# Optimization experiments

Hardware: AMD Instinct MI355X
Metric: run time of the kernel (lower is better)

The kernel has to match this reference:

```python
import jax, jax.numpy as jnp
import numpy as np

H = 4  # num_heads

def _ln(x, g, b):
    m = x.mean(-1, keepdims=True)
    v = ((x - m) ** 2).mean(-1, keepdims=True)
    return (x - m) * jax.lax.rsqrt(v + 1e-5) * g + b

def _mlp(x, w1, b1, w2, b2):
    return jax.nn.relu(x @ w1 + b1) @ w2 + b2

def _lin_att(q, k, v):
    # q,k,v: [BB, L, H, hd] ; linear (kernelized) attention, no softmax
    L = q.shape[1]
    qn = q / jnp.maximum(jnp.linalg.norm(q, axis=-1, keepdims=True), 1e-12)
    kn = k / jnp.maximum(jnp.linalg.norm(k, axis=-1, keepdims=True), 1e-12)
    kvs = jnp.einsum('blhm,blhd->bhmd', kn, v)
    num = jnp.einsum('bnhm,bhmd->bnhd', qn, kvs) + L * v
    den = jnp.einsum('bnhm,bhm->bnh', qn, kn.sum(axis=1))[..., None] + L
    return num / den

def _fast_attn(x4, w_qkv, w_op, b_op):
    # x4: [B,T,N,D]; spatial attention over N, temporal attention over T, concat, project
    B, T, N, D = x4.shape
    hd = D // H
    q, k, v = jnp.split(x4 @ w_qkv, 3, axis=-1)
    sh = lambda t: t.reshape(B * T, N, H, hd)
    out_s = _lin_att(sh(q), sh(k), sh(v)).reshape(B, T, N, D)
    th = lambda t: jnp.swapaxes(t, 1, 2).reshape(B * N, T, H, hd)
    out_t = jnp.swapaxes(_lin_att(th(q), th(k), th(v)).reshape(B, N, T, D), 1, 2)
    return jnp.concatenate([out_s, out_t], axis=-1) @ w_op + b_op

def _forward(x, W_in, b_in, adp, W_tp, b_tp, qkv_w, op_w, op_b, pw_w, pw_b,
             fc_w1, fc_b1, fc_w2, fc_b2, ln1_g, ln1_b, ln2_g, ln2_b,
             ep_w, ep_b, enc_w1, enc_b1, enc_w2, enc_b2, out_w, out_b):
    Nn, T, _ = x.shape
    xt = jnp.swapaxes(x, 0, 1)[None]                 # [1,T,N,in]
    h = xt @ W_in + b_in                             # input_proj -> [1,T,N,24]
    h = jnp.concatenate([h, adp[None]], axis=-1)     # + adaptive emb -> [1,T,N,104]
    h = h @ W_tp + b_tp                              # temporal_proj: 1x1 conv == pointwise linear
    graph = jnp.einsum('tnd,tmd->tnm', adp, adp)     # [T,N,N]
    graph = jax.nn.softmax(jax.nn.relu(graph), axis=-1)  # AvgPool(1,1) is identity
    # GraphPropagate (order=2, eval/no-dropout): [h, graph @ h]
    z1 = jnp.einsum('tni,btid->btnd', graph, h)
    att0 = _fast_attn(h, qkv_w[0], op_w[0], op_b[0])
    att1 = _fast_attn(z1, qkv_w[1], op_w[1], op_b[1])
    # scale = [1, 0.01]; note torch's in-place aliasing makes ln1 input = 2*x_glo
    g = h + att0 * (h @ pw_w[0] + pw_b[0]) + 0.01 * att1 * (att0 @ pw_w[1] + pw_b[1])
    h1 = _ln(2.0 * g, ln1_g, ln1_b)
    h2 = _ln(h1 + _mlp(h1, fc_w1, fc_b1, fc_w2, fc_b2), ln2_g, ln2_b)
    y = jnp.swapaxes(h2, 1, 2).reshape(1, Nn, T * h2.shape[-1]) @ ep_w + ep_b  # encoder_proj
    for i in range(enc_w1.shape[0]):                 # 3 residual MLP blocks
        y = y + _mlp(y, enc_w1[i], enc_b1[i], enc_w2[i], enc_b2[i])
    out = y @ out_w + out_b                          # [1,N,365]
    return out.reshape(Nn, T, 1)

def setup_inputs() -> dict:
    key = jax.random.key(0)
    ks = jax.random.split(key, 24)
    f = lambda i, shape, s=0.05: jax.random.normal(ks[i], shape, dtype=jnp.float32) * s
    D, T, N, IN = 104, 365, 400, 3
    return {
        'x': jax.random.normal(ks[0], (N, T, IN), dtype=jnp.float32),
        'W_in': f(1, (IN, 24)), 'b_in': f(2, (24,)),
        'adp': f(3, (T, N, 80)),
        'W_tp': f(4, (D, D)), 'b_tp': f(5, (D,)),
        'qkv_w': f(6, (2, D, 3 * D)),
        'op_w': f(7, (2, 2 * D, D)), 'op_b': f(8, (2, D)),
        'pw_w': f(9, (2, D, D)), 'pw_b': f(10, (2, D)),
        'fc_w1': f(11, (D, 2 * D)), 'fc_b1': f(12, (2 * D,)),
        'fc_w2': f(13, (2 * D, D)), 'fc_b2': f(14, (D,)),
        'ln1_g': jnp.ones((D,), jnp.float32), 'ln1_b': jnp.zeros((D,), jnp.float32),
        'ln2_g': jnp.ones((D,), jnp.float32), 'ln2_b': jnp.zeros((D,), jnp.float32),
        'ep_w': f(15, (T * D, D), 0.01), 'ep_b': f(16, (D,)),
        'enc_w1': f(17, (3, D, 2 * D)), 'enc_b1': f(18, (3, 2 * D)),
        'enc_w2': f(19, (3, 2 * D, D)), 'enc_b2': f(20, (3, D)),
        'out_w': f(21, (D, T)), 'out_b': f(22, (T,)),
    }

def reference(x, W_in, b_in, adp, W_tp, b_tp, qkv_w, op_w, op_b, pw_w, pw_b,
              fc_w1, fc_b1, fc_w2, fc_b2, ln1_g, ln1_b, ln2_g, ln2_b,
              ep_w, ep_b, enc_w1, enc_b1, enc_w2, enc_b2, out_w, out_b):
    return _forward(x, W_in, b_in, adp, W_tp, b_tp, qkv_w, op_w, op_b, pw_w, pw_b,
                    fc_w1, fc_b1, fc_w2, fc_b2, ln1_g, ln1_b, ln2_g, ln2_b,
                    ep_w, ep_b, enc_w1, enc_b1, enc_w2, enc_b2, out_w, out_b)
```

## Files before the change

kernel.cpp:

```cpp
#include <hip/hip_runtime.h>
#include <hip/hip_bf16.h>
#include <cstddef>

#define TT   365
#define NN   400
#define TN   (TT*NN)
#define HD   26
#define NH   4

#define CEILDIV(a,b) (((a)+(b)-1)/(b))

typedef __hip_bfloat16 bf16;
typedef short short8v __attribute__((ext_vector_type(8)));
typedef float float4v __attribute__((ext_vector_type(4)));
typedef float float16v __attribute__((ext_vector_type(16)));
__device__ __forceinline__ float b2f(bf16 v){ return __bfloat162float(v); }
__device__ __forceinline__ bf16  f2b(float v){ return __float2bfloat16(v); }

static constexpr size_t NB0 = (size_t)TN*104;
static constexpr size_t NB1 = (size_t)TN*104;
static constexpr size_t NB2 = (size_t)TN*312;
static constexpr size_t NB3 = (size_t)TN*104;
static constexpr size_t NBF = NB0+NB1+NB2+NB3;
static constexpr size_t NTILE   = (size_t)108*32;
static constexpr size_t NKVSB_S = (size_t)TT*NTILE;
static constexpr size_t NKVSB_T = (size_t)NN*NTILE;
static constexpr size_t NY      = (size_t)NN*104;
static constexpr size_t NW_TP   = 104*128;
static constexpr size_t NW_QKV  = 312*128;
static constexpr size_t NW_OP   = 104*224;
static constexpr size_t NW_PW   = 104*128;
static constexpr size_t NW_FC1  = 208*128;
static constexpr size_t NW_FC2  = 104*224;
static constexpr size_t NW_EPT  = (size_t)104*37960;
static constexpr size_t NWT     = NW_TP + 2*NW_QKV + 2*NW_OP + 2*NW_PW + NW_FC1 + NW_FC2 + NW_EPT;
static constexpr size_t WS_NEEDED = NBF*2 + (NKVSB_S+NKVSB_T)*2 + NY*4 + NWT*2;
static constexpr size_t NADP_ROWS = (size_t)TN + 64;
static constexpr size_t NADP = NADP_ROWS*96;
static constexpr size_t NHT  = ((size_t)TT*104 + 8)*448;
static_assert(NADP + NHT <= NB2, "z1 scratch must fit in B2");

__global__ void __launch_bounds__(256) prep_w(
    const float* __restrict__ W, bf16* __restrict__ Wt, int K, int Nc, int KP)
{
    int idx = blockIdx.x*256 + threadIdx.x;
    if (idx >= Nc*KP) return;
    int n = idx / KP, k = idx - n*KP;
    Wt[idx] = (k < K) ? f2b(W[(size_t)k*Nc + n]) : f2b(0.f);
}

__global__ void __launch_bounds__(256) prep_wT(
    const float* __restrict__ W, bf16* __restrict__ Wt)
{
    __shared__ float T[64][105];
    int k0 = blockIdx.x * 64;
    int tid = threadIdx.x;
    for (int idx = tid; idx < 64*104; idx += 256) {
        int r = idx / 104, c = idx - r*104;
        int k = k0 + r;
        T[r][c] = (k < 37960) ? W[(size_t)k*104 + c] : 0.f;
    }
    __syncthreads();
    for (int idx = tid; idx < 104*32; idx += 256) {
        int n = idx >> 5, kp = idx & 31;
        int k = kp*2;
        if (k0 + k + 1 < 37960 || k0 + k < 37960) {
            if (k0 + k < 37960) {
                bf16 lo = f2b(T[k][n]);
                bf16 hi = f2b(T[k+1][n]);
                uint v = ((uint)(*(ushort*)&hi) << 16) | (*(ushort*)&lo);
                if (k0 + k + 1 < 37960) *(uint*)(Wt + (size_t)n*37960 + k0 + k) = v;
                else Wt[(size_t)n*37960 + k0 + k] = lo;
            }
        }
    }
}

__global__ void __launch_bounds__(256) prep_adp(
    const float* __restrict__ adp, bf16* __restrict__ out)
{
    size_t i = (size_t)blockIdx.x*256 + threadIdx.x;
    if (i >= NADP) return;
    size_t row = i / 96; int e = (int)(i - row*96);
    float v = (row < TN && e < 80) ? adp[row*80 + e] : 0.f;
    out[i] = f2b(v);
}

__global__ void __launch_bounds__(256) ht_kernel(
    const bf16* __restrict__ h, bf16* __restrict__ hT)
{
    __shared__ bf16 As[64*106];
    int t = blockIdx.y, n0 = blockIdx.x*64;
    int tid = threadIdx.x;
    for (int idx = tid; idx < 64*52; idx += 256) {
        int r = idx / 52, k = idx - r*52;
        int n = n0 + r;
        uint v = 0;
        if (n < NN) v = *(const uint*)(h + ((size_t)t*NN + n)*104 + k*2);
        *(uint*)(&As[r*106 + k*2]) = v;
    }
    __syncthreads();
    for (int idx = tid; idx < 104*32; idx += 256) {
        int d = idx >> 5, np = idx & 31;
        int n = np*2;
        ushort lo = *(ushort*)&As[n*106 + d];
        ushort hi = *(ushort*)&As[(n+1)*106 + d];
        uint v = ((uint)hi << 16) | lo;
        *(uint*)(hT + ((size_t)t*104 + d)*448 + n0 + n) = v;
    }
}

__global__ void __launch_bounds__(128) hcat_kernel(
    const float* __restrict__ x, const float* __restrict__ W_in,
    const float* __restrict__ b_in, const float* __restrict__ adp,
    bf16* __restrict__ hcat)
{
    int bid = blockIdx.x;
    int t = bid / NN, n = bid - t*NN;
    int tid = threadIdx.x;
    if (tid < 24) {
        float s = b_in[tid];
        size_t xb = ((size_t)n*TT + t)*3;
        #pragma unroll
        for (int i = 0; i < 3; ++i) s += x[xb + i] * W_in[i*24 + tid];
        hcat[(size_t)bid*104 + tid] = f2b(s);
    } else if (tid < 104) {
        hcat[(size_t)bid*104 + tid] = f2b(adp[(size_t)bid*80 + (tid - 24)]);
    }
}

template<int KP>
__global__ void __launch_bounds__(256) gemm_mf(
    const bf16* __restrict__ A, int lda, int K,
    const bf16* __restrict__ Wt, const float* __restrict__ bias,
    bf16* __restrict__ C, int M, int Nc, int relu)
{
    constexpr int STR = KP + 8;
    constexpr int KPQ = KP/8;
    __shared__ bf16 As[64*STR];
    __shared__ bf16 Ws[64*STR];
    int nCol = (Nc + 63) >> 6;
    int nwg = gridDim.x;
    int bid = blockIdx.x;
    int xcd = bid & 7, kk = bid >> 3;
    int q8 = nwg >> 3, r8 = nwg & 7;
    int widx = (xcd < r8 ? xcd*(q8+1) : r8*(q8+1) + (xcd - r8)*q8) + kk;
    int mblk = widx / nCol;
    int m0 = mblk * 64;
    int c0 = (widx - mblk*nCol) * 64;
    int tid = threadIdx.x;
    const int KQ = K/8;
    uint4 z4 = {0u,0u,0u,0u};
    for (int idx = tid; idx < 64*KPQ; idx += 256) {
        int r = idx / KPQ, q = idx - r*KPQ;
        int m = m0 + r;
        uint4 v = z4;
        if (m < M && q < KQ) v = *(const uint4*)(A + (size_t)m*lda + q*8);
        *(uint4*)(&As[r*STR + q*8]) = v;
    }
    for (int idx = tid; idx < 64*KPQ; idx += 256) {
        int r = idx / KPQ, q = idx - r*KPQ;
        int n = c0 + r;
        uint4 v = z4;
        if (n < Nc) v = *(const uint4*)(Wt + (size_t)n*KP + q*8);
        *(uint4*)(&Ws[r*STR + q*8]) = v;
    }
    __syncthreads();

    int lane = tid & 63, w = tid >> 6;
    int n16 = lane & 15, quad = lane >> 4;
    constexpr int KS = KP/32;
    short8v af[KS];
    #pragma unroll
    for (int s = 0; s < KS; ++s)
        af[s] = *(const short8v*)(&As[(16*w + n16)*STR + s*32 + quad*8]);
    float4v acc[4];
    #pragma unroll
    for (int ct = 0; ct < 4; ++ct) { float4v z = {0.f,0.f,0.f,0.f}; acc[ct] = z; }
    #pragma unroll
    for (int ct = 0; ct < 4; ++ct) {
        #pragma unroll
        for (int s = 0; s < KS; ++s) {
            short8v bfr = *(const short8v*)(&Ws[(ct*16 + n16)*STR + s*32 + quad*8]);
            acc[ct] = __builtin_amdgcn_mfma_f32_16x16x32_bf16(af[s], bfr, acc[ct], 0, 0, 0);
        }
    }
    #pragma unroll
    for (int ct = 0; ct < 4; ++ct) {
        int c = c0 + ct*16 + n16;
        if (c < Nc) {
            float b = bias ? bias[c] : 0.f;
            #pragma unroll
            for (int reg = 0; reg < 4; ++reg) {
                int m = m0 + 16*w + quad*4 + reg;
                if (m < M) {
                    float v = acc[ct][reg] + b;
                    if (relu) v = fmaxf(v, 0.f);
                    C[(size_t)m*Nc + c] = f2b(v);
                }
            }
        }
    }
}

__global__ void __launch_bounds__(256) gate_ln1(
    bf16* __restrict__ h, const bf16* __restrict__ att0, const bf16* __restrict__ att1,
    const bf16* __restrict__ w0t, const bf16* __restrict__ w1t, const float* __restrict__ pwb,
    const float* __restrict__ gamma, const float* __restrict__ beta)
{
    constexpr int STR = 136;
    __shared__ bf16 A0s[64*STR];
    __shared__ bf16 A1s[64*STR];
    __shared__ bf16 Ws[112*STR];
    __shared__ float prm[416];
    int m0 = blockIdx.x * 64;
    int tid = threadIdx.x;
    int lane = tid & 63, w = tid >> 6, n16 = lane & 15, quad = lane >> 4;
    uint4 z4 = {0u,0u,0u,0u};

    for (int idx = tid; idx < 64*16; idx += 256) {
        int r = idx >> 4, q = idx & 15;
        int m = m0 + r;
        uint4 v0 = z4, v1 = z4;
        if (m < TN && q < 13) {
            v0 = *(const uint4*)(h    + (size_t)m*104 + q*8);
            v1 = *(const uint4*)(att0 + (size_t)m*104 + q*8);
        }
        *(uint4*)(&A0s[r*STR + q*8]) = v0;
        *(uint4*)(&A1s[r*STR + q*8]) = v1;
    }
    for (int idx = tid; idx < 112*16; idx += 256) {
        int c = idx >> 4, q = idx & 15;
        uint4 v = z4;
        if (c < 104) v = *(const uint4*)(w0t + (size_t)c*128 + q*8);
        *(uint4*)(&Ws[c*STR + q*8]) = v;
    }
    for (int i = tid; i < 416; i += 256)
        prm[i] = (i < 208) ? pwb[i] : (i < 312 ? gamma[i-208] : beta[i-312]);
    __syncthreads();

    short8v a0f[4], a1f[4];
    #pragma unroll
    for (int s = 0; s < 4; ++s) {
        a0f[s] = *(const short8v*)(&A0s[(16*w + n16)*STR + s*32 + quad*8]);
        a1f[s] = *(const short8v*)(&A1s[(16*w + n16)*STR + s*32 + quad*8]);
    }
    float4v acc0[7], acc1[7];
    #pragma unroll
    for (int ct = 0; ct < 7; ++ct) { float4v z = {0.f,0.f,0.f,0.f}; acc0[ct] = z; acc1[ct] = z; }
    #pragma unroll
    for (int ct = 0; ct < 7; ++ct)
        #pragma unroll
        for (int s = 0; s < 4; ++s) {
            short8v bfr = *(const short8v*)(&Ws[(ct*16 + n16)*STR + s*32 + quad*8]);
            acc0[ct] = __builtin_amdgcn_mfma_f32_16x16x32_bf16(a0f[s], bfr, acc0[ct], 0, 0, 0);
        }
    __syncthreads();
    for (int idx = tid; idx < 112*16; idx += 256) {
        int c = idx >> 4, q = idx & 15;
        uint4 v = z4;
        if (c < 104) v = *(const uint4*)(w1t + (size_t)c*128 + q*8);
        *(uint4*)(&Ws[c*STR + q*8]) = v;
    }
    __syncthreads();
    #pragma unroll
    for (int ct = 0; ct < 7; ++ct)
        #pragma unroll
        for (int s = 0; s < 4; ++s) {
            short8v bfr = *(const short8v*)(&Ws[(ct*16 + n16)*STR + s*32 + quad*8]);
            acc1[ct] = __builtin_amdgcn_mfma_f32_16x16x32_bf16(a1f[s], bfr, acc1[ct], 0, 0, 0);
        }

    float sum[4] = {0.f,0.f,0.f,0.f};
    #pragma unroll
    for (int ct = 0; ct < 7; ++ct) {
        int c = ct*16 + n16;
        bool colok = c < 104;
        float b0 = colok ? prm[c] : 0.f;
        float b1 = colok ? prm[104 + c] : 0.f;
        #pragma unroll
        for (int reg = 0; reg < 4; ++reg) {
            int r = 16*w + quad*4 + reg;
            int m = m0 + r;
            float xv = 0.f;
            if (colok && m < TN) {
                float p0 = acc0[ct][reg] + b0;
                float p1 = acc1[ct][reg] + b1;
                float hv = b2f(A0s[r*STR + c]);
                float a0 = b2f(A1s[r*STR + c]);
                float a1 = b2f(att1[(size_t)m*104 + c]);
                xv = 2.f*(hv + a0*p0 + 0.01f*a1*p1);
            }
            acc0[ct][reg] = xv;
            sum[reg] += xv;
        }
    }
    #pragma unroll
    for (int reg = 0; reg < 4; ++reg) {
        float v = sum[reg];
        v += __shfl_xor(v,1,64); v += __shfl_xor(v,2,64);
        v += __shfl_xor(v,4,64); v += __shfl_xor(v,8,64);
        sum[reg] = v * (1.f/104.f);
    }
    float var[4] = {0.f,0.f,0.f,0.f};
    #pragma unroll
    for (int ct = 0; ct < 7; ++ct) {
        bool colok = (ct*16 + n16) < 104;
        #pragma unroll
        for (int reg = 0; reg < 4; ++reg) {
            if (colok) {
                float d = acc0[ct][reg] - sum[reg];
                acc0[ct][reg] = d;
                var[reg] += d*d;
            }
        }
    }
    #pragma unroll
    for (int reg = 0; reg < 4; ++reg) {
        float v = var[reg];
        v += __shfl_xor(v,1,64); v += __shfl_xor(v,2,64);
        v += __shfl_xor(v,4,64); v += __shfl_xor(v,8,64);
        var[reg] = rsqrtf(v * (1.f/104.f) + 1e-5f);
    }
    #pragma unroll
    for (int ct = 0; ct < 7; ++ct) {
        int c = ct*16 + n16;
        if (c < 104) {
            float g = prm[208 + c], be = prm[312 + c];
            #pragma unroll
            for (int reg = 0; reg < 4; ++reg) {
                int m = m0 + 16*w + quad*4 + reg;
                if (m < TN)
                    h[(size_t)m*104 + c] = f2b(acc0[ct][reg]*var[reg]*g + be);
            }
        }
    }
}

__global__ void __launch_bounds__(256) fc2_ln2(
    const bf16* __restrict__ hidden, const bf16* __restrict__ w2t, const float* __restrict__ b2,
    const bf16* __restrict__ h1, const float* __restrict__ gamma, const float* __restrict__ beta,
    bf16* __restrict__ h2)
{
    constexpr int STRA = 232;
    constexpr int STRW = 136;
    __shared__ bf16 As[64*STRA];
    __shared__ bf16 Ws[112*STRW];
    __shared__ float prm[312];
    int m0 = blockIdx.x * 64;
    int tid = threadIdx.x;
    int lane = tid & 63, w = tid >> 6, n16 = lane & 15, quad = lane >> 4;
    uint4 z4 = {0u,0u,0u,0u};

    for (int idx = tid; idx < 64*28; idx += 256) {
        int r = idx / 28, q = idx - r*28;
        int m = m0 + r;
        uint4 v = z4;
        if (m < TN && q < 26) v = *(const uint4*)(hidden + (size_t)m*208 + q*8);
        *(uint4*)(&As[r*STRA + q*8]) = v;
    }
    for (int idx = tid; idx < 112*16; idx += 256) {
        int c = idx >> 4, q = idx & 15;
        uint4 v = z4;
        if (c < 104) v = *(const uint4*)(w2t + (size_t)c*224 + q*8);
        *(uint4*)(&Ws[c*STRW + q*8]) = v;
    }
    for (int i = tid; i < 312; i += 256)
        prm[i] = (i < 104) ? b2[i] : (i < 208 ? gamma[i-104] : beta[i-208]);
    __syncthreads();

    short8v af[7];
    #pragma unroll
    for (int s = 0; s < 7; ++s)
        af[s] = *(const short8v*)(&As[(16*w + n16)*STRA + s*32 + quad*8]);
    float4v acc[7];
    #pragma unroll
    for (int ct = 0; ct < 7; ++ct) { float4v z = {0.f,0.f,0.f,0.f}; acc[ct] = z; }
    #pragma unroll
    for (int ct = 0; ct < 7; ++ct)
        #pragma unroll
        for (int s = 0; s < 4; ++s) {
            short8v bfr = *(const short8v*)(&Ws[(ct*16 + n16)*STRW + s*32 + quad*8]);
            acc[ct] = __builtin_amdgcn_mfma_f32_16x16x32_bf16(af[s], bfr, acc[ct], 0, 0, 0);
        }
    __syncthreads();
    for (int idx = tid; idx < 112*16; idx += 256) {
        int c = idx >> 4, q = idx & 15;
        uint4 v = z4;
        if (c < 104 && q < 12) v = *(const uint4*)(w2t + (size_t)c*224 + 128 + q*8);
        *(uint4*)(&Ws[c*STRW + q*8]) = v;
    }
    __syncthreads();
    #pragma unroll
    for (int ct = 0; ct < 7; ++ct)
        #pragma unroll
        for (int s = 4; s < 7; ++s) {
            short8v bfr = *(const short8v*)(&Ws[(ct*16 + n16)*STRW + (s-4)*32 + quad*8]);
            acc[ct] = __builtin_amdgcn_mfma_f32_16x16x32_bf16(af[s], bfr, acc[ct], 0, 0, 0);
        }

    float sum[4] = {0.f,0.f,0.f,0.f};
    #pragma unroll
    for (int ct = 0; ct < 7; ++ct) {
        int c = ct*16 + n16;
        bool colok = c < 104;
        float bb = colok ? prm[c] : 0.f;
        #pragma unroll
        for (int reg = 0; reg < 4; ++reg) {
            int m = m0 + 16*w + quad*4 + reg;
            float xv = 0.f;
            if (colok && m < TN)
                xv = b2f(h1[(size_t)m*104 + c]) + acc[ct][reg] + bb;
            acc[ct][reg] = xv;
            sum[reg] += xv;
        }
    }
    #pragma unroll
    for (int reg = 0; reg < 4; ++reg) {
        float v = sum[reg];
        v += __shfl_xor(v,1,64); v += __shfl_xor(v,2,64);
        v += __shfl_xor(v,4,64); v += __shfl_xor(v,8,64);
        sum[reg] = v * (1.f/104.f);
    }
    float var[4] = {0.f,0.f,0.f,0.f};
    #pragma unroll
    for (int ct = 0; ct < 7; ++ct) {
        bool colok = (ct*16 + n16) < 104;
        #pragma unroll
        for (int reg = 0; reg < 4; ++reg) {
            if (colok) {
                float d = acc[ct][reg] - sum[reg];
                acc[ct][reg] = d;
                var[reg] += d*d;
            }
        }
    }
    #pragma unroll
    for (int reg = 0; reg < 4; ++reg) {
        float v = var[reg];
        v += __shfl_xor(v,1,64); v += __shfl_xor(v,2,64);
        v += __shfl_xor(v,4,64); v += __shfl_xor(v,8,64);
        var[reg] = rsqrtf(v * (1.f/104.f) + 1e-5f);
    }
    #pragma unroll
    for (int ct = 0; ct < 7; ++ct) {
        int c = ct*16 + n16;
        if (c < 104) {
            float g = prm[104 + c], be = prm[208 + c];
            #pragma unroll
            for (int reg = 0; reg < 4; ++reg) {
                int m = m0 + 16*w + quad*4 + reg;
                if (m < TN)
                    h2[(size_t)m*104 + c] = f2b(acc[ct][reg]*var[reg]*g + be);
            }
        }
    }
}

__global__ void __launch_bounds__(256) ep_mf(
    const bf16* __restrict__ h2, const bf16* __restrict__ wt, float* __restrict__ y)
{
    constexpr int STR = 136;
    __shared__ bf16 As[64*STR];
    __shared__ bf16 Ws[64*STR];
    int m0 = blockIdx.x * 64;
    int c0 = blockIdx.y * 64;
    int t0 = blockIdx.z * 8;
    int t1 = min(TT, t0 + 8);
    int tid = threadIdx.x;
    int lane = tid & 63, w = tid >> 6, n16 = lane & 15, quad = lane >> 4;
    uint4 z4 = {0u,0u,0u,0u};

    float4v acc[4];
    #pragma unroll
    for (int ct = 0; ct < 4; ++ct) { float4v z = {0.f,0.f,0.f,0.f}; acc[ct] = z; }

    for (int t = t0; t < t1; ++t) {
        for (int idx = tid; idx < 64*16; idx += 256) {
            int r = idx >> 4, q = idx & 15;
            int m = m0 + r;
            uint4 va = z4;
            if (m < NN && q < 13) va = *(const uint4*)(h2 + ((size_t)t*NN + m)*104 + q*8);
            *(uint4*)(&As[r*STR + q*8]) = va;
            int c = c0 + r;
            uint4 vw = z4;
            if (c < 104 && q < 13) vw = *(const uint4*)(wt + (size_t)c*37960 + t*104 + q*8);
            *(uint4*)(&Ws[r*STR + q*8]) = vw;
        }
        __syncthreads();
        short8v af[4];
        #pragma unroll
        for (int s = 0; s < 4; ++s)
            af[s] = *(const short8v*)(&As[(16*w + n16)*STR + s*32 + quad*8]);
        #pragma unroll
        for (int ct = 0; ct < 4; ++ct) {
            #pragma unroll
            for (int s = 0; s < 4; ++s) {
                short8v bfr = *(const short8v*)(&Ws[(ct*16 + n16)*STR + s*32 + quad*8]);
                acc[ct] = __builtin_amdgcn_mfma_f32_16x16x32_bf16(af[s], bfr, acc[ct], 0, 0, 0);
            }
        }
        __syncthreads();
    }
    #pragma unroll
    for (int ct = 0; ct < 4; ++ct) {
        int c = c0 + ct*16 + n16;
        if (c < 104) {
            #pragma unroll
            for (int reg = 0; reg < 4; ++reg) {
                int m = m0 + 16*w + quad*4 + reg;
                if (m < NN) atomicAdd(&y[(size_t)m*104 + c], acc[ct][reg]);
            }
        }
    }
}

static constexpr int Z1_TQ = CEILDIV(TT, 8);
static constexpr int Z1_BLOCKS = 8 * Z1_TQ * 4;
__global__ void __launch_bounds__(512, 4) z1_mf(
    const bf16* __restrict__ adp_bf, const bf16* __restrict__ hT, bf16* __restrict__ z1)
{
    constexpr int SA  = 104;
    constexpr int SH  = 72;
    constexpr int SPP = 72;
    __shared__ bf16 Asq[2][64*SA];
    __shared__ bf16 Bt[64*SA];
    __shared__ bf16 Hs[128*SH];
    __shared__ bf16 P[2][64*SPP];
    __shared__ float rsb[2][2][64];

    int bid = blockIdx.x;
    int xcd = bid & 7;
    int j = bid >> 3;
    int tq = j >> 2, pair = j & 3;
    int t = tq*8 + xcd;
    if (t >= TT) return;

    int tid = threadIdx.x;
    int lane = tid & 63, w = tid >> 6;
    int slab = w >> 2, wsl = w & 3;
    int qi = wsl >> 1, ci = wsl & 1;
    int n32 = lane & 31, koct = lane >> 5;
    int r0 = (pair*2 + slab)*64;

    {
        const uint4* src = (const uint4*)(adp_bf + ((size_t)t*NN + pair*128)*96);
        #pragma unroll
        for (int i = 0; i < 3; ++i) {
            int idx = tid + i*512;
            int s2 = idx / 768, rem = idx - s2*768;
            int r = rem / 12, q = rem - r*12;
            *(uint4*)(&Asq[s2][r*SA + q*8]) = src[idx];
        }
    }
    {
        uint4 z4v = {0u,0u,0u,0u};
        for (int idx = tid; idx < 216; idx += 512) {
            int rr = idx / 9;
            int r = 104 + rr, q = idx - rr*9;
            *(uint4*)(&Hs[r*SH + q*8]) = z4v;
        }
    }

    float16v on0, on1;
    #pragma unroll
    for (int i = 0; i < 16; ++i) { on0[i] = 0.f; on1[i] = 0.f; }
    float rs2[16];
    #pragma unroll
    for (int i = 0; i < 16; ++i) rs2[i] = 0.f;

    const bf16* hbase = hT + (size_t)t*104*448;

    uint4 preB0, preB1, preH0, preH1;
    {
        const uint4* srcB = (const uint4*)(adp_bf + (size_t)t*NN*96);
        preB0 = srcB[tid];
        if (tid < 256) preB1 = srcB[tid + 512];
        { int r = tid >> 3, q = tid & 7;
          preH0 = *(const uint4*)(hbase + (size_t)r*448 + q*8); }
        if (tid < 320) { int idx = tid + 512; int r = idx >> 3, q = idx & 7;
          preH1 = *(const uint4*)(hbase + (size_t)r*448 + q*8); }
    }

    for (int c0 = 0; c0 < NN; c0 += 64) {
        { int r = tid / 12, q = tid - (tid/12)*12;
          *(uint4*)(&Bt[r*SA + q*8]) = preB0; }
        if (tid < 256) { int idx = tid + 512; int r = idx / 12, q = idx - r*12;
          *(uint4*)(&Bt[r*SA + q*8]) = preB1; }
        { int r = tid >> 3, q = tid & 7;
          *(uint4*)(&Hs[r*SH + q*8]) = preH0; }
        if (tid < 320) { int idx = tid + 512; int r = idx >> 3, q = idx & 7;
          *(uint4*)(&Hs[r*SH + q*8]) = preH1; }
        __syncthreads();
        int cn = c0 + 64;
        if (cn < NN) {
            const uint4* srcB = (const uint4*)(adp_bf + ((size_t)t*NN + cn)*96);
            preB0 = srcB[tid];
            if (tid < 256) preB1 = srcB[tid + 512];
            { int r = tid >> 3, q = tid & 7;
              preH0 = *(const uint4*)(hbase + (size_t)r*448 + cn + q*8); }
            if (tid < 320) { int idx = tid + 512; int r = idx >> 3, q = idx & 7;
              preH1 = *(const uint4*)(hbase + (size_t)r*448 + cn + q*8); }
        }
        float16v sc;
        #pragma unroll
        for (int i = 0; i < 16; ++i) sc[i] = 0.f;
        #pragma unroll
        for (int s = 0; s < 6; ++s) {
            short8v afq = *(const short8v*)(&Asq[slab][(qi*32 + n32)*SA + s*16 + koct*8]);
            short8v bfr = *(const short8v*)(&Bt[(ci*32 + n32)*SA + s*16 + koct*8]);
            sc = __builtin_amdgcn_mfma_f32_32x32x16_bf16(afq, bfr, sc, 0, 0, 0);
        }
        bool colok = (c0 + ci*32 + n32) < NN;
        #pragma unroll
        for (int reg = 0; reg < 16; ++reg) {
            int crow = (reg & 3) + 8*(reg >> 2) + 4*koct;
            float e = colok ? __expf(fmaxf(sc[reg], 0.f)) : 0.f;
            rs2[reg] += e;
            P[slab][(qi*32 + crow)*SPP + ci*32 + n32] = f2b(e);
        }
        __syncthreads();
        short8v pA[4];
        #pragma unroll
        for (int s = 0; s < 4; ++s)
            pA[s] = *(const short8v*)(&P[slab][(qi*32 + n32)*SPP + s*16 + koct*8]);
        #pragma unroll
        for (int s = 0; s < 4; ++s) {
            short8v hb0 = *(const short8v*)(&Hs[(ci*32 + n32)*SH + s*16 + koct*8]);
            on0 = __builtin_amdgcn_mfma_f32_32x32x16_bf16(pA[s], hb0, on0, 0, 0, 0);
        }
        #pragma unroll
        for (int s = 0; s < 4; ++s) {
            short8v hb1 = *(const short8v*)(&Hs[((ci+2)*32 + n32)*SH + s*16 + koct*8]);
            on1 = __builtin_amdgcn_mfma_f32_32x32x16_bf16(pA[s], hb1, on1, 0, 0, 0);
        }
        __syncthreads();
    }

    #pragma unroll
    for (int reg = 0; reg < 16; ++reg) {
        float v = rs2[reg];
        v += __shfl_xor(v, 1, 64);
        v += __shfl_xor(v, 2, 64);
        v += __shfl_xor(v, 4, 64);
        v += __shfl_xor(v, 8, 64);
        v += __shfl_xor(v, 16, 64);
        if (n32 == 0) {
            int crow = (reg & 3) + 8*(reg >> 2) + 4*koct;
            rsb[slab][ci][qi*32 + crow] = v;
        }
    }
    __syncthreads();

    #pragma unroll
    for (int reg = 0; reg < 16; ++reg) {
        int crow = (reg & 3) + 8*(reg >> 2) + 4*koct;
        int qrow = qi*32 + crow;
        int gq = r0 + qrow;
        if (gq < NN) {
            float inv = 1.f / (rsb[slab][0][qrow] + rsb[slab][1][qrow]);
            int d0 = ci*32 + n32;
            z1[((size_t)t*NN + gq)*104 + d0] = f2b(on0[reg] * inv);
            int d1 = (ci + 2)*32 + n32;
            if (d1 < 104)
                z1[((size_t)t*NN + gq)*104 + d1] = f2b(on1[reg] * inv);
        }
    }
}

__global__ void __launch_bounds__(256) kvs_mf(
    const bf16* __restrict__ qkv, bf16* __restrict__ kvsb_s, bf16* __restrict__ kvsb_t)
{
    constexpr int CK = 32;
    constexpr int TS = 40;
    __shared__ bf16 raw[CK][216];
    __shared__ bf16 kTn[4][32][TS];
    __shared__ bf16 vT [4][32][TS];
    __shared__ float invs[CK][4];

    int bb = blockIdx.x;
    bf16* out; int L; long long strideL, base;
    if (bb < TT) { out = kvsb_s + (size_t)bb*NTILE; L = NN; base = (long long)bb*NN*312 + 104; strideL = 312; }
    else { int n = bb - TT; out = kvsb_t + (size_t)n*NTILE; L = TT; base = (long long)n*312 + 104; strideL = (long long)NN*312; }

    int tid = threadIdx.x;
    int lane = tid & 63, w = tid >> 6;
    int n32 = lane & 31, koct = lane >> 5;
    uint4 z4 = {0u,0u,0u,0u};

    float16v acc;
    #pragma unroll
    for (int i = 0; i < 16; ++i) acc[i] = 0.f;

    uint4 pre[4];
    #pragma unroll
    for (int j = 0; j < 4; ++j) {
        int idx = tid + j*256;
        uint4 v = z4;
        if (idx < CK*26) {
            int r = idx / 26, q = idx - r*26;
            if (r < L) v = *(const uint4*)(qkv + base + (long long)r*strideL + q*8);
        }
        pre[j] = v;
    }

    for (int l0 = 0; l0 < L; l0 += CK) {
        int lw = min(CK, L - l0);
        __syncthreads();
        #pragma unroll
        for (int j = 0; j < 4; ++j) {
            int idx = tid + j*256;
            if (idx < CK*26) {
                int r = idx / 26, q = idx - r*26;
                *(uint4*)(&raw[r][q*8]) = pre[j];
            }
        }
        __syncthreads();
        {
            int ln0 = l0 + CK;
            #pragma unroll
            for (int j = 0; j < 4; ++j) {
                int idx = tid + j*256;
                uint4 v = z4;
                if (idx < CK*26 && ln0 < L) {
                    int r = idx / 26, q = idx - r*26;
                    if (r < L - ln0) v = *(const uint4*)(qkv + base + (long long)(ln0 + r)*strideL + q*8);
                }
                pre[j] = v;
            }
        }
        if (tid < CK*4) {
            int l = tid >> 2, h = tid & 3;
            float ss = 0.f;
            #pragma unroll
            for (int m = 0; m < HD; ++m) { float v = b2f(raw[l][h*HD + m]); ss += v*v; }
            invs[l][h] = (l < lw) ? 1.f/fmaxf(sqrtf(ss), 1e-12f) : 0.f;
        }
        __syncthreads();
        for (int idx = tid; idx < 4*CK*HD; idx += 256) {
            int h = idx / (CK*HD); int rem = idx - h*CK*HD;
            int l = rem / HD; int m = rem - l*HD;
            float iv = invs[l][h];
            kTn[h][m][l] = f2b(b2f(raw[l][h*HD + m]) * iv);
            vT[h][m][l]  = raw[l][104 + h*HD + m];
        }
        if (tid < 4*CK) {
            int h = tid >> 5, l = tid & 31;
            vT[h][26][l] = f2b((l < lw) ? 1.f : 0.f);
        }
        __syncthreads();
        #pragma unroll
        for (int s = 0; s < 2; ++s) {
            short8v a = *(const short8v*)(&kTn[w][n32][s*16 + koct*8]);
            short8v b = *(const short8v*)(&vT [w][n32][s*16 + koct*8]);
            acc = __builtin_amdgcn_mfma_f32_32x32x16_bf16(a, b, acc, 0, 0, 0);
        }
    }

    int lo = w*HD;
    #pragma unroll
    for (int reg = 0; reg < 16; ++reg) {
        int m = (reg & 3) + 8*(reg >> 2) + 4*koct;
        if (m < HD) {
            if (n32 < HD)       out[(size_t)(lo + n32)*32 + m] = f2b(acc[reg]);
            else if (n32 == HD) out[(size_t)(104 + w)*32 + m] = f2b(acc[reg]);
        }
    }
}

__global__ void __launch_bounds__(256) attn_mm(
    bf16* __restrict__ qkv, const bf16* __restrict__ kvsb,
    int M, long long bStride, long long rowStride, float Lf, int outOff)
{
    constexpr int STR = 136;
    __shared__ bf16 As[64*STR];
    __shared__ bf16 Ws[112*STR];
    __shared__ float nsqL[64*4];
    __shared__ float denL[64*4];
    int mt = blockIdx.x, bb = blockIdx.y;
    int tid = threadIdx.x;
    int lane = tid & 63, w = tid >> 6, n16 = lane & 15, quad = lane >> 4;
    bf16* base = qkv + (size_t)bb * bStride;
    int r0 = mt*64;
    uint4 z4 = {0u,0u,0u,0u};

    for (int idx = tid; idx < 64*16; idx += 256) {
        int r = idx >> 4, q = idx & 15;
        int m = r0 + r;
        uint4 v = z4;
        if (m < M && q < 13) v = *(const uint4*)(base + (size_t)m*rowStride + q*8);
        *(uint4*)(&As[r*STR + q*8]) = v;
    }
    for (int idx = tid; idx < 112*16; idx += 256) {
        int c = idx >> 4, q = idx & 15;
        *(uint4*)(&Ws[c*STR + q*8]) = z4;
    }
    __syncthreads();
    {
        const bf16* kb = kvsb + (size_t)bb * NTILE;
        for (int idx = tid; idx < 108*13; idx += 256) {
            int c = idx / 13, qu = idx - c*13;
            int lo = (c < 104) ? (c/26)*26 : (c-104)*26;
            *(uint*)(&Ws[c*STR + lo + qu*2]) = *(const uint*)(kb + (size_t)c*32 + qu*2);
        }
    }
    __syncthreads();

    short8v af[4];
    #pragma unroll
    for (int s = 0; s < 4; ++s)
        af[s] = *(const short8v*)(&As[(16*w + n16)*STR + s*32 + quad*8]);
    float4v acc[7];
    #pragma unroll
    for (int ct = 0; ct < 7; ++ct) { float4v z = {0.f,0.f,0.f,0.f}; acc[ct] = z; }
    #pragma unroll
    for (int ct = 0; ct < 7; ++ct) {
        #pragma unroll
        for (int s = 0; s < 4; ++s) {
            short8v bfr = *(const short8v*)(&Ws[(ct*16 + n16)*STR + s*32 + quad*8]);
            acc[ct] = __builtin_amdgcn_mfma_f32_16x16x32_bf16(af[s], bfr, acc[ct], 0, 0, 0);
        }
    }
    {
        int row = tid >> 2, hh = tid & 3;
        const bf16* qr = &As[row*STR + hh*26];
        float ss = 0.f;
        #pragma unroll
        for (int m = 0; m < HD; ++m) { float v = b2f(qr[m]); ss += v*v; }
        nsqL[row*4 + hh] = ss;
    }
    if (n16 >= 8 && n16 < 12) {
        #pragma unroll
        for (int reg = 0; reg < 4; ++reg)
            denL[(16*w + quad*4 + reg)*4 + (n16 - 8)] = acc[6][reg];
    }
    __syncthreads();
    #pragma unroll
    for (int ct = 0; ct < 7; ++ct) {
        int c = ct*16 + n16;
        if (c < 104) {
            int hh = c / 26;
            #pragma unroll
            for (int reg = 0; reg < 4; ++reg) {
                int lr = 16*w + quad*4 + reg;
                int m = r0 + lr;
                if (m < M) {
                    float iq = 1.f / fmaxf(sqrtf(nsqL[lr*4 + hh]), 1e-12f);
                    float den = iq * denL[lr*4 + hh] + Lf;
                    bf16* rp = base + (size_t)m*rowStride;
                    float num = iq * acc[ct][reg] + Lf * b2f(rp[208 + c]);
                    rp[outOff + c] = f2b(num / den);
                }
            }
        }
    }
}

__global__ void __launch_bounds__(256) y_init_kernel(float* __restrict__ y, const float* __restrict__ ep_b) {
    int i = blockIdx.x*256 + threadIdx.x;
    if (i < NN*104) y[i] = ep_b[i % 104];
}

__global__ void __launch_bounds__(256) enc_kernel(
    float* __restrict__ y, const float* __restrict__ w1, const float* __restrict__ b1,
    const float* __restrict__ w2, const float* __restrict__ b2)
{
    int n = blockIdx.x;
    int tid = threadIdx.x;
    __shared__ float yr[104], hid[208];
    if (tid < 104) yr[tid] = y[(size_t)n*104 + tid];
    __syncthreads();
    if (tid < 208) {
        float s = b1[tid];
        for (int k = 0; k < 104; ++k) s += yr[k] * w1[(size_t)k*208 + tid];
        hid[tid] = fmaxf(s, 0.f);
    }
    __syncthreads();
    if (tid < 104) {
        float s = b2[tid];
        for (int k = 0; k < 208; ++k) s += hid[k] * w2[(size_t)k*104 + tid];
        y[(size_t)n*104 + tid] = yr[tid] + s;
    }
}

__global__ void __launch_bounds__(256) out_kernel(
    const float* __restrict__ y, const float* __restrict__ out_w,
    const float* __restrict__ out_b, float* __restrict__ out)
{
    int n = blockIdx.x;
    int tid = threadIdx.x;
    __shared__ float yr[104];
    if (tid < 104) yr[tid] = y[(size_t)n*104 + tid];
    __syncthreads();
    for (int t = tid; t < TT; t += 256) {
        float s = out_b[t];
        for (int d = 0; d < 104; ++d) s += yr[d] * out_w[(size_t)d*TT + t];
        out[(size_t)n*TT + t] = s;
    }
}

extern "C" void kernel_launch(void* const* d_in, const int* in_sizes, int n_in,
                              void* d_out, int out_size, void* d_ws, size_t ws_size,
                              hipStream_t stream) {
    if (ws_size < WS_NEEDED) return;

    const float* x      = (const float*)d_in[0];
    const float* W_in   = (const float*)d_in[1];
    const float* b_in   = (const float*)d_in[2];
    const float* adp    = (const float*)d_in[3];
    const float* W_tp   = (const float*)d_in[4];
    const float* b_tp   = (const float*)d_in[5];
    const float* qkv_w  = (const float*)d_in[6];
    const float* op_w   = (const float*)d_in[7];
    const float* op_b   = (const float*)d_in[8];
    const float* pw_w   = (const float*)d_in[9];
    const float* pw_b   = (const float*)d_in[10];
    const float* fc_w1  = (const float*)d_in[11];
    const float* fc_b1  = (const float*)d_in[12];
    const float* fc_w2  = (const float*)d_in[13];
    const float* fc_b2  = (const float*)d_in[14];
    const float* ln1_g  = (const float*)d_in[15];
    const float* ln1_b  = (const float*)d_in[16];
    const float* ln2_g  = (const float*)d_in[17];
    const float* ln2_b  = (const float*)d_in[18];
    const float* ep_w   = (const float*)d_in[19];
    const float* ep_b   = (const float*)d_in[20];
    const float* enc_w1 = (const float*)d_in[21];
    const float* enc_b1 = (const float*)d_in[22];
    const float* enc_w2 = (const float*)d_in[23];
    const float* enc_b2 = (const float*)d_in[24];
    const float* out_w  = (const float*)d_in[25];
    const float* out_b  = (const float*)d_in[26];

    bf16* B0 = (bf16*)d_ws;
    bf16* B1 = B0 + NB0;
    bf16* B2 = B1 + NB1;
    bf16* B3 = B2 + NB2;
    bf16* kvsb_s = B3 + NB3;
    bf16* kvsb_t = kvsb_s + NKVSB_S;
    float* ybuf  = (float*)(kvsb_t + NKVSB_T);
    bf16* wtp   = (bf16*)(ybuf + NY);
    bf16* wqkv0 = wtp + NW_TP;
    bf16* wqkv1 = wqkv0 + NW_QKV;
    bf16* wop0  = wqkv1 + NW_QKV;
    bf16* wop1  = wop0 + NW_OP;
    bf16* wpw0  = wop1 + NW_OP;
    bf16* wpw1  = wpw0 + NW_PW;
    bf16* wfc1  = wpw1 + NW_PW;
    bf16* wfc2  = wfc1 + NW_FC1;
    bf16* wept  = wfc2 + NW_FC2;
    bf16* adp_bf = B2;
    bf16* hTbuf  = B2 + NADP;

    prep_w<<<CEILDIV(104*128,256), 256, 0, stream>>>(W_tp, wtp, 104, 104, 128);
    prep_w<<<CEILDIV(312*128,256), 256, 0, stream>>>(qkv_w, wqkv0, 104, 312, 128);
    prep_w<<<CEILDIV(312*128,256), 256, 0, stream>>>(qkv_w + 104*312, wqkv1, 104, 312, 128);
    prep_w<<<CEILDIV(104*224,256), 256, 0, stream>>>(op_w, wop0, 208, 104, 224);
    prep_w<<<CEILDIV(104*224,256), 256, 0, stream>>>(op_w + 208*104, wop1, 208, 104, 224);
    prep_w<<<CEILDIV(104*128,256), 256, 0, stream>>>(pw_w, wpw0, 104, 104, 128);
    prep_w<<<CEILDIV(104*128,256), 256, 0, stream>>>(pw_w + 104*104, wpw1, 104, 104, 128);
    prep_w<<<CEILDIV(208*128,256), 256, 0, stream>>>(fc_w1, wfc1, 104, 208, 128);
    prep_w<<<CEILDIV(104*224,256), 256, 0, stream>>>(fc_w2, wfc2, 208, 104, 224);
    prep_wT<<<CEILDIV(37960,64), 256, 0, stream>>>(ep_w, wept);

    const int GX = CEILDIV(TN, 64);

    hcat_kernel<<<TN, 128, 0, stream>>>(x, W_in, b_in, adp, B2);
    gemm_mf<128><<<GX*2, 256, 0, stream>>>(B2, 104, 104, wtp, b_tp, B0, TN, 104, 0);
    prep_adp<<<CEILDIV((int)NADP,256), 256, 0, stream>>>(adp, adp_bf);
    ht_kernel<<<dim3(7, TT), 256, 0, stream>>>(B0, hTbuf);
    z1_mf<<<Z1_BLOCKS, 512, 0, stream>>>(adp_bf, hTbuf, B1);
    gemm_mf<128><<<GX*5, 256, 0, stream>>>(B0, 104, 104, wqkv0, nullptr, B2, TN, 312, 0);
    kvs_mf<<<TT+NN, 256, 0, stream>>>(B2, kvsb_s, kvsb_t);
    attn_mm<<<dim3(6, NN), 256, 0, stream>>>(B2, kvsb_t, TT, 312, (long long)NN*312, (float)TT, 104);
    attn_mm<<<dim3(7, TT), 256, 0, stream>>>(B2, kvsb_s, NN, (long long)NN*312, 312, (float)NN, 0);
    gemm_mf<224><<<GX*2, 256, 0, stream>>>(B2, 312, 208, wop0, op_b, B3, TN, 104, 0);
    gemm_mf<128><<<GX*5, 256, 0, stream>>>(B1, 104, 104, wqkv1, nullptr, B2, TN, 312, 0);
    kvs_mf<<<TT+NN, 256, 0, stream>>>(B2, kvsb_s, kvsb_t);
    attn_mm<<<dim3(6, NN), 256, 0, stream>>>(B2, kvsb_t, TT, 312, (long long)NN*312, (float)TT, 104);
    attn_mm<<<dim3(7, TT), 256, 0, stream>>>(B2, kvsb_s, NN, (long long)NN*312, 312, (float)NN, 0);
    gemm_mf<224><<<GX*2, 256, 0, stream>>>(B2, 312, 208, wop1, op_b + 104, B1, TN, 104, 0);
    gate_ln1<<<GX, 256, 0, stream>>>(B0, B3, B1, wpw0, wpw1, pw_b, ln1_g, ln1_b);
    gemm_mf<128><<<GX*4, 256, 0, stream>>>(B0, 104, 104, wfc1, fc_b1, B2, TN, 208, 1);
    fc2_ln2<<<GX, 256, 0, stream>>>(B2, wfc2, fc_b2, B0, ln2_g, ln2_b, B3);
    y_init_kernel<<<CEILDIV(NN*104,256), 256, 0, stream>>>(ybuf, ep_b);
    ep_mf<<<dim3(CEILDIV(NN,64), 2, CEILDIV(TT,8)), 256, 0, stream>>>(B3, wept, ybuf);
    for (int i = 0; i < 3; ++i)
        enc_kernel<<<NN, 256, 0, stream>>>(ybuf, enc_w1 + (size_t)i*104*208, enc_b1 + (size_t)i*208,
                                           enc_w2 + (size_t)i*208*104, enc_b2 + (size_t)i*104);
    out_kernel<<<NN, 256, 0, stream>>>(ybuf, out_w, out_b, (float*)d_out);
}
```

Measured before the change: 1.303 ms.

## Use 128x128 MFMA GEMM tiles, batch hcat rows, fuse encoder and output tail

Adds a gemm_mf2 kernel with 128x128 output tiles, four 64x64 warp subtiles and launch bounds of 2 blocks per CU. It replaces the 64x64 GEMMs for the temporal projection, both QKV projections and fc1, which cuts redundant weight and activation loads to LDS. hcat now handles 16 rows per block staged through shared memory with vectorized 16-byte stores, instead of one row per block. The three encoder launches and the output kernel are fused into a single tail kernel that keeps y in shared memory. Risks are higher register and LDS pressure and lower occupancy in the larger-tile GEMM.

```diff
diff --git a/kernel.cpp b/kernel.cpp
--- a/kernel.cpp
+++ b/kernel.cpp
@@ -110,22 +110,30 @@
     }
 }
 
-__global__ void __launch_bounds__(128) hcat_kernel(
+__global__ void __launch_bounds__(256) hcat_kernel(
     const float* __restrict__ x, const float* __restrict__ W_in,
     const float* __restrict__ b_in, const float* __restrict__ adp,
     bf16* __restrict__ hcat)
 {
-    int bid = blockIdx.x;
-    int t = bid / NN, n = bid - t*NN;
-    int tid = threadIdx.x;
-    if (tid < 24) {
-        float s = b_in[tid];
+    __shared__ bf16 T[16][112];
+    int r0 = blockIdx.x * 16;
+    int tid = threadIdx.x;
+    for (int idx = tid; idx < 16*24; idx += 256) {
+        int r = idx / 24, c = idx - r*24;
+        int row = r0 + r;
+        int t = row / NN, n = row - t*NN;
         size_t xb = ((size_t)n*TT + t)*3;
-        #pragma unroll
-        for (int i = 0; i < 3; ++i) s += x[xb + i] * W_in[i*24 + tid];
-        hcat[(size_t)bid*104 + tid] = f2b(s);
-    } else if (tid < 104) {
-        hcat[(size_t)bid*104 + tid] = f2b(adp[(size_t)bid*80 + (tid - 24)]);
+        float s = b_in[c] + x[xb]*W_in[c] + x[xb+1]*W_in[24+c] + x[xb+2]*W_in[48+c];
+        T[r][c] = f2b(s);
+    }
+    for (int idx = tid; idx < 16*80; idx += 256) {
+        int r = idx / 80, e = idx - r*80;
+        T[r][24+e] = f2b(adp[(size_t)(r0+r)*80 + e]);
+    }
+    __syncthreads();
+    for (int idx = tid; idx < 16*13; idx += 256) {
+        int r = idx / 13, q = idx - r*13;
+        *(uint4*)(hcat + ((size_t)(r0+r))*104 + q*8) = *(const uint4*)(&T[r][q*8]);
     }
 }
 
@@ -197,6 +205,89 @@
                     float v = acc[ct][reg] + b;
                     if (relu) v = fmaxf(v, 0.f);
                     C[(size_t)m*Nc + c] = f2b(v);
+                }
+            }
+        }
+    }
+}
+
+template<int KP>
+__global__ void __launch_bounds__(256, 2) gemm_mf2(
+    const bf16* __restrict__ A, int lda, int K,
+    const bf16* __restrict__ Wt, const float* __restrict__ bias,
+    bf16* __restrict__ C, int M, int Nc, int relu)
+{
+    constexpr int STR = KP + 8;
+    constexpr int KPQ = KP/8;
+    __shared__ bf16 As[128*STR];
+    __shared__ bf16 Ws[128*STR];
+    int nCol = (Nc + 127) >> 7;
+    int nwg = gridDim.x;
+    int bid = blockIdx.x;
+    int xcd = bid & 7, kk = bid >> 3;
+    int q8 = nwg >> 3, r8 = nwg & 7;
+    int widx = (xcd < r8 ? xcd*(q8+1) : r8*(q8+1) + (xcd - r8)*q8) + kk;
+    int mblk = widx / nCol;
+    int m0 = mblk * 128;
+    int c0 = (widx - mblk*nCol) * 128;
+    int tid = threadIdx.x;
+    const int KQ = K/8;
+    uint4 z4 = {0u,0u,0u,0u};
+    for (int idx = tid; idx < 128*KPQ; idx += 256) {
+        int r = idx / KPQ, q = idx - r*KPQ;
+        int m = m0 + r;
+        uint4 v = z4;
+        if (m < M && q < KQ) v = *(const uint4*)(A + (size_t)m*lda + q*8);
+        *(uint4*)(&As[r*STR + q*8]) = v;
+    }
+    for (int idx = tid; idx < 128*KPQ; idx += 256) {
+        int r = idx / KPQ, q = idx - r*KPQ;
+        int n = c0 + r;
+        uint4 v = z4;
+        if (n < Nc) v = *(const uint4*)(Wt + (size_t)n*KP + q*8);
+        *(uint4*)(&Ws[r*STR + q*8]) = v;
+    }
+    __syncthreads();
+
+    int lane = tid & 63, w = tid >> 6;
+    int wr = (w >> 1)*64, wc = (w & 1)*64;
+    int n16 = lane & 15, quad = lane >> 4;
+    constexpr int KS = KP/32;
+    float4v acc[4][4];
+    #pragma unroll
+    for (int mt = 0; mt < 4; ++mt)
+        #pragma unroll
+        for (int ct = 0; ct < 4; ++ct) { float4v z = {0.f,0.f,0.f,0.f}; acc[mt][ct] = z; }
+    #pragma unroll
+    for (int mt = 0; mt < 4; ++mt) {
+        short8v af[KS];
+        #pragma unroll
+        for (int s = 0; s < KS; ++s)
+            af[s] = *(const short8v*)(&As[(wr + mt*16 + n16)*STR + s*32 + quad*8]);
+        #pragma unroll
+        for (int ct = 0; ct < 4; ++ct) {
+            #pragma unroll
+            for (int s = 0; s < KS; ++s) {
+                short8v bfr = *(const short8v*)(&Ws[(wc + ct*16 + n16)*STR + s*32 + quad*8]);
+                acc[mt][ct] = __builtin_amdgcn_mfma_f32_16x16x32_bf16(af[s], bfr, acc[mt][ct], 0, 0, 0);
+            }
+        }
+    }
+    #pragma unroll
+    for (int ct = 0; ct < 4; ++ct) {
+        int c = c0 + wc + ct*16 + n16;
+        if (c < Nc) {
+            float b = bias ? bias[c] : 0.f;
+            #pragma unroll
+            for (int mt = 0; mt < 4; ++mt) {
+                #pragma unroll
+                for (int reg = 0; reg < 4; ++reg) {
+                    int m = m0 + wr + mt*16 + quad*4 + reg;
+                    if (m < M) {
+                        float v = acc[mt][ct][reg] + b;
+                        if (relu) v = fmaxf(v, 0.f);
+                        C[(size_t)m*Nc + c] = f2b(v);
+                    }
                 }
             }
         }
@@ -861,37 +952,39 @@
     if (i < NN*104) y[i] = ep_b[i % 104];
 }
 
-__global__ void __launch_bounds__(256) enc_kernel(
-    float* __restrict__ y, const float* __restrict__ w1, const float* __restrict__ b1,
-    const float* __restrict__ w2, const float* __restrict__ b2)
+__global__ void __launch_bounds__(256) tail_kernel(
+    const float* __restrict__ y,
+    const float* __restrict__ ew1, const float* __restrict__ eb1,
+    const float* __restrict__ ew2, const float* __restrict__ eb2,
+    const float* __restrict__ out_w, const float* __restrict__ out_b,
+    float* __restrict__ out)
 {
     int n = blockIdx.x;
     int tid = threadIdx.x;
     __shared__ float yr[104], hid[208];
     if (tid < 104) yr[tid] = y[(size_t)n*104 + tid];
     __syncthreads();
-    if (tid < 208) {
-        float s = b1[tid];
-        for (int k = 0; k < 104; ++k) s += yr[k] * w1[(size_t)k*208 + tid];
-        hid[tid] = fmaxf(s, 0.f);
-    }
-    __syncthreads();
-    if (tid < 104) {
-        float s = b2[tid];
-        for (int k = 0; k < 208; ++k) s += hid[k] * w2[(size_t)k*104 + tid];
-        y[(size_t)n*104 + tid] = yr[tid] + s;
-    }
-}
-
-__global__ void __launch_bounds__(256) out_kernel(
-    const float* __restrict__ y, const float* __restrict__ out_w,
-    const float* __restrict__ out_b, float* __restrict__ out)
-{
-    int n = blockIdx.x;
-    int tid = threadIdx.x;
-    __shared__ float yr[104];
-    if (tid < 104) yr[tid] = y[(size_t)n*104 + tid];
-    __syncthreads();
+    for (int i = 0; i < 3; ++i) {
+        const float* w1 = ew1 + (size_t)i*104*208;
+        const float* b1 = eb1 + (size_t)i*208;
+        const float* w2 = ew2 + (size_t)i*208*104;
+        const float* b2 = eb2 + (size_t)i*104;
+        if (tid < 208) {
+            float s = b1[tid];
+            for (int k = 0; k < 104; ++k) s += yr[k] * w1[(size_t)k*208 + tid];
+            hid[tid] = fmaxf(s, 0.f);
+        }
+        __syncthreads();
+        float ynew = 0.f;
+        if (tid < 104) {
+            float s = b2[tid];
+            for (int k = 0; k < 208; ++k) s += hid[k] * w2[(size_t)k*104 + tid];
+            ynew = yr[tid] + s;
+        }
+        __syncthreads();
+        if (tid < 104) yr[tid] = ynew;
+        __syncthreads();
+    }
     for (int t = tid; t < TT; t += 256) {
         float s = out_b[t];
         for (int d = 0; d < 104; ++d) s += yr[d] * out_w[(size_t)d*TT + t];
@@ -963,30 +1056,29 @@
     prep_w<<<CEILDIV(104*224,256), 256, 0, stream>>>(fc_w2, wfc2, 208, 104, 224);
     prep_wT<<<CEILDIV(37960,64), 256, 0, stream>>>(ep_w, wept);
 
-    const int GX = CEILDIV(TN, 64);
-
-    hcat_kernel<<<TN, 128, 0, stream>>>(x, W_in, b_in, adp, B2);
-    gemm_mf<128><<<GX*2, 256, 0, stream>>>(B2, 104, 104, wtp, b_tp, B0, TN, 104, 0);
+    const int GX  = CEILDIV(TN, 64);
+    const int GM2 = CEILDIV(TN, 128);
+
+    hcat_kernel<<<CEILDIV(TN,16), 256, 0, stream>>>(x, W_in, b_in, adp, B2);
+    gemm_mf2<128><<<GM2, 256, 0, stream>>>(B2, 104, 104, wtp, b_tp, B0, TN, 104, 0);
     prep_adp<<<CEILDIV((int)NADP,256), 256, 0, stream>>>(adp, adp_bf);
     ht_kernel<<<dim3(7, TT), 256, 0, stream>>>(B0, hTbuf);
     z1_mf<<<Z1_BLOCKS, 512, 0, stream>>>(adp_bf, hTbuf, B1);
-    gemm_mf<128><<<GX*5, 256, 0, stream>>>(B0, 104, 104, wqkv0, nullptr, B2, TN, 312, 0);
+    gemm_mf2<128><<<GM2*3, 256, 0, stream>>>(B0, 104, 104, wqkv0, nullptr, B2, TN, 312, 0);
     kvs_mf<<<TT+NN, 256, 0, stream>>>(B2, kvsb_s, kvsb_t);
     attn_mm<<<dim3(6, NN), 256, 0, stream>>>(B2, kvsb_t, TT, 312, (long long)NN*312, (float)TT, 104);
     attn_mm<<<dim3(7, TT), 256, 0, stream>>>(B2, kvsb_s, NN, (long long)NN*312, 312, (float)NN, 0);
     gemm_mf<224><<<GX*2, 256, 0, stream>>>(B2, 312, 208, wop0, op_b, B3, TN, 104, 0);
-    gemm_mf<128><<<GX*5, 256, 0, stream>>>(B1, 104, 104, wqkv1, nullptr, B2, TN, 312, 0);
+    gemm_mf2<128><<<GM2*3, 256, 0, stream>>>(B1, 104, 104, wqkv1, nullptr, B2, TN, 312, 0);
     kvs_mf<<<TT+NN, 256, 0, stream>>>(B2, kvsb_s, kvsb_t);
     attn_mm<<<dim3(6, NN), 256, 0, stream>>>(B2, kvsb_t, TT, 312, (long long)NN*312, (float)TT, 104);
     attn_mm<<<dim3(7, TT), 256, 0, stream>>>(B2, kvsb_s, NN, (long long)NN*312, 312, (float)NN, 0);
     gemm_mf<224><<<GX*2, 256, 0, stream>>>(B2, 312, 208, wop1, op_b + 104, B1, TN, 104, 0);
     gate_ln1<<<GX, 256, 0, stream>>>(B0, B3, B1, wpw0, wpw1, pw_b, ln1_g, ln1_b);
-    gemm_mf<128><<<GX*4, 256, 0, stream>>>(B0, 104, 104, wfc1, fc_b1, B2, TN, 208, 1);
+    gemm_mf2<128><<<GM2*2, 256, 0, stream>>>(B0, 104, 104, wfc1, fc_b1, B2, TN, 208, 1);
     fc2_ln2<<<GX, 256, 0, stream>>>(B2, wfc2, fc_b2, B0, ln2_g, ln2_b, B3);
     y_init_kernel<<<CEILDIV(NN*104,256), 256, 0, stream>>>(ybuf, ep_b);
     ep_mf<<<dim3(CEILDIV(NN,64), 2, CEILDIV(TT,8)), 256, 0, stream>>>(B3, wept, ybuf);
-    for (int i = 0; i < 3; ++i)
-        enc_kernel<<<NN, 256, 0, stream>>>(ybuf, enc_w1 + (size_t)i*104*208, enc_b1 + (size_t)i*208,
-                                           enc_w2 + (size_t)i*208*104, enc_b2 + (size_t)i*104);
-    out_kernel<<<NN, 256, 0, stream>>>(ybuf, out_w, out_b, (float*)d_out);
-}
+    tail_kernel<<<NN, 256, 0, stream>>>(ybuf, enc_w1, enc_b1, enc_w2, enc_b2,
+                                        out_w, out_b, (float*)d_out);
+}
```

After: 1.363 ms. +4.6%, slower.
